# Optimization experiments

Measured on AMD Instinct MI355X. Metric: run time of the kernel, lower is better.

## Reference

```python
import jax, jax.numpy as jnp
import numpy as np

B, L, H = 2, 4096, 1024
ED, N, R, K = 2048, 16, 64, 4


def setup_inputs() -> dict:
    key = jax.random.key(0)
    ks = jax.random.split(key, 8)
    w = lambda i, shape, s=0.02: jax.random.normal(ks[i], shape, jnp.float32) * s
    # dt bias initialized like Mamba: inv-softplus of dt ~ logU(1e-3, 1e-1)
    dt = jnp.exp(jax.random.uniform(ks[7], (ED,)) * (np.log(0.1) - np.log(0.001)) + np.log(0.001))
    dt = jnp.clip(dt, 1e-4)
    inv_dt = dt + jnp.log(-jnp.expm1(-dt))
    A = jnp.broadcast_to(jnp.arange(1, N + 1, dtype=jnp.float32), (ED, N))
    return dict(
        x=jax.random.normal(ks[0], (B, L, H), jnp.float32),
        in_proj_w=w(1, (2 * ED, H)),
        conv_w=w(2, (ED, K), 0.2),
        conv_b=jnp.zeros((ED,), jnp.float32),
        x_proj_w=w(3, (R + 2 * N, ED)),
        dt_w=w(4, (ED, R), 64 ** -0.5),
        dt_b=inv_dt,
        A_log=jnp.log(A),
        D=jnp.ones((ED,), jnp.float32),
        out_proj_w=w(5, (H, ED)),
    )


def reference(x, in_proj_w, conv_w, conv_b, x_proj_w, dt_w, dt_b, A_log, D, out_proj_w):
    Bq, Lq, Hq = x.shape
    EDq, Kq = conv_w.shape
    Rq = dt_w.shape[1]
    Nq = A_log.shape[1]

    # in_proj -> [B, L, 2*ED]; chunk into hidden_states and gate
    xz = jnp.einsum('blh,eh->ble', x, in_proj_w)
    hs, gate = jnp.split(xz, 2, axis=-1)

    # causal depthwise conv1d along L (padding K-1 on the left), then SiLU
    hs_pad = jnp.pad(hs, ((0, 0), (Kq - 1, 0), (0, 0)))  # [B, L+K-1, ED]
    conv = conv_b
    for k in range(Kq):  # K=4, fixed small loop
        conv = conv + hs_pad[:, k:k + Lq, :] * conv_w[:, k]
    hs = jax.nn.silu(conv)  # [B, L, ED]

    # x_proj -> split into dt (rank R), B (N), C (N)
    ssm = jnp.einsum('ble,pe->blp', hs, x_proj_w)
    dtr, Bm, Cm = jnp.split(ssm, [Rq, Rq + Nq], axis=-1)

    # dt_proj + softplus (delta_softplus=True with delta_bias)
    delta = jax.nn.softplus(jnp.einsum('blr,er->ble', dtr, dt_w) + dt_b)  # [B,L,ED]

    A = -jnp.exp(A_log)  # [ED, N]

    # selective scan: h_t = exp(delta_t*A)*h_{t-1} + delta_t*B_t*u_t ; y_t = <h_t, C_t>
    def step(h, inp):
        d_t, B_t, C_t, u_t = inp  # [B,ED], [B,N], [B,N], [B,ED]
        dA = jnp.exp(d_t[..., None] * A)                      # [B,ED,N]
        h = dA * h + (d_t * u_t)[..., None] * B_t[:, None, :]  # [B,ED,N]
        y = jnp.einsum('ben,bn->be', h, C_t)                   # [B,ED]
        return h, y

    h0 = jnp.zeros((Bq, EDq, Nq), x.dtype)
    xs = (jnp.moveaxis(delta, 1, 0), jnp.moveaxis(Bm, 1, 0),
          jnp.moveaxis(Cm, 1, 0), jnp.moveaxis(hs, 1, 0))
    _, ys = jax.lax.scan(step, h0, xs)  # ys: [L, B, ED]

    y = jnp.moveaxis(ys, 0, 1) + hs * D      # skip term D*u
    y = y * jax.nn.silu(gate)                # gated output
    return jnp.einsum('ble,he->blh', y, out_proj_w)
```

## Files before the change

### kernel.cpp

```cpp
#include <hip/hip_runtime.h>


typedef float f32x4 __attribute__((ext_vector_type(4)));
typedef short short8 __attribute__((ext_vector_type(8)));

#define DEV __device__ __forceinline__

DEV float bf2f(unsigned short u) {
  union { unsigned int i; float f; } v; v.i = ((unsigned int)u) << 16; return v.f;
}
DEV unsigned short f2bf(float f) {
  union { float f; unsigned int i; } v; v.f = f;
  return (unsigned short)((v.i + 0x7fffu + ((v.i >> 16) & 1u)) >> 16);
}

DEV void gload_lds16(const void* g, void* l) {
  __builtin_amdgcn_global_load_lds(
      (const __attribute__((address_space(1))) unsigned int*)g,
      (__attribute__((address_space(3))) unsigned int*)l, 16, 0, 0);
}

DEV void mfma_bf16(f32x4& d, short8 a, short8 b) {
  asm("v_mfma_f32_16x16x32_bf16 %0, %1, %2, %0" : "+v"(d) : "v"(a), "v"(b));
}

template <int BM, int BN, int WM, int WN, int EPI>
__global__ __launch_bounds__(256) void gemm_bt_kernel(
    const unsigned short* __restrict__ A, const unsigned short* __restrict__ Bw,
    int M, int N, int Kd,
    float* __restrict__ o_f32, unsigned short* __restrict__ o_b16a,
    unsigned short* __restrict__ o_b16b, const float* __restrict__ bias,
    float* __restrict__ oB, float* __restrict__ oC)
{
  constexpr int MFR = BM / WM / 16;
  constexpr int NFR = BN / WN / 16;
  constexpr int TA = BM * 4;
  constexpr int TB = BN * 4;
  __shared__ unsigned short lds[(BM + BN) * 32];

  const int tid  = threadIdx.x;
  const int wave = tid >> 6;
  const int lane = tid & 63;
  const int row  = lane & 15;
  const int g    = lane >> 4;
  const int swz  = g ^ ((row >> 1) & 3);
  const int rowBase = blockIdx.y * BM;
  const int colBase = blockIdx.x * BN;
  const int WROW = (wave / WN) * (BM / WM);
  const int WCOL = (wave % WN) * (BN / WN);

  f32x4 acc[MFR][NFR];
  const f32x4 fz = {0.f, 0.f, 0.f, 0.f};
#pragma unroll
  for (int i = 0; i < MFR; ++i)
#pragma unroll
    for (int j = 0; j < NFR; ++j) acc[i][j] = fz;

  for (int kk = 0; kk < Kd; kk += 32) {
#pragma unroll
    for (int c0 = 0; c0 < TA; c0 += 256) {
      int ch = c0 + tid;
      if (ch < TA) {
        int r = ch >> 2;
        int gs = (ch & 3) ^ ((r >> 1) & 3);
        gload_lds16(A + (size_t)(rowBase + r) * Kd + kk + gs * 8,
                    (void*)(lds + (c0 + wave * 64) * 8));
      }
    }
#pragma unroll
    for (int c0 = 0; c0 < TB; c0 += 256) {
      int ch = c0 + tid;
      if (ch < TB) {
        int r = ch >> 2;
        int gs = (ch & 3) ^ ((r >> 1) & 3);
        gload_lds16(Bw + (size_t)(colBase + r) * Kd + kk + gs * 8,
                    (void*)(lds + BM * 32 + (c0 + wave * 64) * 8));
      }
    }
    __syncthreads();
    short8 af[MFR], bfr[NFR];
#pragma unroll
    for (int mi = 0; mi < MFR; ++mi)
      af[mi] = *(const short8*)(lds + (WROW + mi * 16 + row) * 32 + swz * 8);
#pragma unroll
    for (int ni = 0; ni < NFR; ++ni)
      bfr[ni] = *(const short8*)(lds + BM * 32 + (WCOL + ni * 16 + row) * 32 + swz * 8);
#pragma unroll
    for (int mi = 0; mi < MFR; ++mi)
#pragma unroll
      for (int ni = 0; ni < NFR; ++ni)
        mfma_bf16(acc[mi][ni], af[mi], bfr[ni]);
    __syncthreads();
  }

#pragma unroll
  for (int mi = 0; mi < MFR; ++mi) {
#pragma unroll
    for (int ni = 0; ni < NFR; ++ni) {
      const int gcol = colBase + WCOL + ni * 16 + row;
#pragma unroll
      for (int r = 0; r < 4; ++r) {
        const int grow = rowBase + WROW + mi * 16 + g * 4 + r;
        float v = acc[mi][ni][r];
        if constexpr (EPI == 0) {
          o_f32[(size_t)grow * N + gcol] = v;
        } else if constexpr (EPI == 1) {
          if (gcol < 2048) o_b16a[(size_t)grow * 2048 + gcol] = f2bf(v);
          else             o_b16b[(size_t)grow * 2048 + (gcol - 2048)] = f2bf(v);
        } else if constexpr (EPI == 2) {
          if (gcol < 64)      o_b16a[(size_t)grow * 64 + gcol] = f2bf(v);
          else if (gcol < 80) oB[(size_t)grow * 16 + (gcol - 64)] = v;
          else                oC[(size_t)grow * 16 + (gcol - 80)] = v;
        } else {
          float x = v + bias[gcol];
          o_f32[(size_t)grow * N + gcol] = (x > 20.f) ? x : __logf(1.f + __expf(x));
        }
      }
    }
  }
}

__global__ __launch_bounds__(256) void cvt_bf16_kernel(
    const float* __restrict__ in, unsigned short* __restrict__ out, int n8)
{
  int i = blockIdx.x * 256 + threadIdx.x;
  if (i >= n8) return;
  const float4* p = (const float4*)(in + (size_t)i * 8);
  float4 a = p[0], b = p[1];
  float v[8] = {a.x, a.y, a.z, a.w, b.x, b.y, b.z, b.w};
  unsigned o[4];
#pragma unroll
  for (int q = 0; q < 4; ++q)
    o[q] = (unsigned)f2bf(v[2 * q]) | ((unsigned)f2bf(v[2 * q + 1]) << 16);
  *(uint4*)(out + (size_t)i * 8) = make_uint4(o[0], o[1], o[2], o[3]);
}

__global__ __launch_bounds__(256) void conv_silu_kernel(
    const unsigned short* __restrict__ hsraw, const float* __restrict__ cw,
    const float* __restrict__ cb, unsigned short* __restrict__ hsb)
{
  int idx = blockIdx.x * 256 + threadIdx.x;
  int e0 = (idx & 255) * 8;
  int t  = (idx >> 8) & 4095;
  int b  = idx >> 20;
  float acc[8];
  float wv[4][8];
#pragma unroll
  for (int j = 0; j < 8; ++j) acc[j] = cb[e0 + j];
#pragma unroll
  for (int k = 0; k < 4; ++k)
#pragma unroll
    for (int j = 0; j < 8; ++j) wv[k][j] = cw[(e0 + j) * 4 + k];
#pragma unroll
  for (int k = 0; k < 4; ++k) {
    int tt = t - 3 + k;
    if (tt < 0) continue;
    uint4 v4 = *(const uint4*)(hsraw + ((size_t)(b * 4096 + tt)) * 2048 + e0);
    unsigned arr[4] = {v4.x, v4.y, v4.z, v4.w};
#pragma unroll
    for (int q = 0; q < 4; ++q) {
      acc[2 * q]     += wv[k][2 * q]     * bf2f((unsigned short)(arr[q] & 0xffffu));
      acc[2 * q + 1] += wv[k][2 * q + 1] * bf2f((unsigned short)(arr[q] >> 16));
    }
  }
  unsigned o[4];
#pragma unroll
  for (int q = 0; q < 4; ++q) {
    float a0 = acc[2 * q], a1 = acc[2 * q + 1];
    a0 = a0 / (1.f + __expf(-a0));
    a1 = a1 / (1.f + __expf(-a1));
    o[q] = (unsigned)f2bf(a0) | ((unsigned)f2bf(a1) << 16);
  }
  *(uint4*)(hsb + ((size_t)(b * 4096 + t)) * 2048 + e0) = make_uint4(o[0], o[1], o[2], o[3]);
}

__global__ __launch_bounds__(256) void scan_phase1(
    const float* __restrict__ delta, const unsigned short* __restrict__ hsb,
    const float* __restrict__ Bb, const float* __restrict__ alog,
    float* __restrict__ h_end, float* __restrict__ Ssum)
{
  __shared__ __align__(16) float Bs[64 * 16];
  const int tid = threadIdx.x;
  const int e = blockIdx.x * 256 + tid;
  const int c = blockIdx.y;
  const int b = blockIdx.z;
  const int t0 = c * 64;
  {
    const float* src = Bb + ((size_t)(b * 4096 + t0)) * 16;
#pragma unroll
    for (int k = 0; k < 4; ++k) Bs[tid + k * 256] = src[tid + k * 256];
  }
  float An[16];
  {
    const float4* ap = (const float4*)(alog + e * 16);
#pragma unroll
    for (int q = 0; q < 4; ++q) {
      float4 v = ap[q];
      An[4*q+0] = -__expf(v.x); An[4*q+1] = -__expf(v.y);
      An[4*q+2] = -__expf(v.z); An[4*q+3] = -__expf(v.w);
    }
  }
  __syncthreads();
  float h[16];
#pragma unroll
  for (int n = 0; n < 16; ++n) h[n] = 0.f;
  float sumd = 0.f;
  size_t base = ((size_t)(b * 4096 + t0)) * 2048 + e;
  float dd = delta[base];
  float uu = bf2f(hsb[base]);
  for (int j = 0; j < 64; ++j) {
    int jn = (j < 63) ? j + 1 : 63;
    float d_nxt = delta[base + (size_t)jn * 2048];
    float u_nxt = bf2f(hsb[base + (size_t)jn * 2048]);
    const float4* Bv = (const float4*)(Bs + j * 16);
    float4 b0 = Bv[0], b1 = Bv[1], b2 = Bv[2], b3 = Bv[3];
    float Bl[16] = {b0.x,b0.y,b0.z,b0.w, b1.x,b1.y,b1.z,b1.w,
                    b2.x,b2.y,b2.z,b2.w, b3.x,b3.y,b3.z,b3.w};
    sumd += dd;
    float du = dd * uu;
#pragma unroll
    for (int n = 0; n < 16; ++n)
      h[n] = fmaf(__expf(An[n] * dd), h[n], du * Bl[n]);
    dd = d_nxt; uu = u_nxt;
  }
  float* he = h_end + (((size_t)(b * 2048 + e)) * 64 + c) * 16;
#pragma unroll
  for (int q = 0; q < 4; ++q) {
    float4 v = {h[4*q], h[4*q+1], h[4*q+2], h[4*q+3]};
    *(float4*)(he + 4 * q) = v;
  }
  Ssum[((size_t)(b * 2048 + e)) * 64 + c] = sumd;
}

__global__ __launch_bounds__(256) void scan_phase2(
    const float* __restrict__ h_end, const float* __restrict__ Ssum,
    const float* __restrict__ alog, float* __restrict__ h_start)
{
  const int tid = threadIdx.x;
  const int n = tid & 15;
  const int G = blockIdx.x * 16 + (tid >> 4);
  const int e = G & 2047;
  const float An = -__expf(alog[e * 16 + n]);
  size_t hb = (size_t)G * 64 * 16 + n;
  size_t sb = (size_t)G * 64;
  float h = 0.f;
  constexpr int PF = 8;
  float hq[PF], Sq[PF];
#pragma unroll
  for (int j = 0; j < PF; ++j) { hq[j] = h_end[hb + (size_t)j * 16]; Sq[j] = Ssum[sb + j]; }
  for (int c0 = 0; c0 < 64; c0 += PF) {
    float hn[PF], Sn[PF];
#pragma unroll
    for (int j = 0; j < PF; ++j) {
      int cn = c0 + PF + j; cn = (cn < 64) ? cn : 63;
      hn[j] = h_end[hb + (size_t)cn * 16]; Sn[j] = Ssum[sb + cn];
    }
#pragma unroll
    for (int j = 0; j < PF; ++j) {
      h_start[hb + (size_t)(c0 + j) * 16] = h;
      h = fmaf(__expf(An * Sq[j]), h, hq[j]);
    }
#pragma unroll
    for (int j = 0; j < PF; ++j) { hq[j] = hn[j]; Sq[j] = Sn[j]; }
  }
}

__global__ __launch_bounds__(256) void scan_phase3(
    const float* __restrict__ delta, const unsigned short* __restrict__ hsb,
    const float* __restrict__ Bb, const float* __restrict__ Cb,
    const float* __restrict__ alog, const float* __restrict__ h_start,
    const float* __restrict__ Dv, unsigned short* __restrict__ gate_y2)
{
  __shared__ __align__(16) float Bs[64 * 16];
  __shared__ __align__(16) float Cs[64 * 16];
  const int tid = threadIdx.x;
  const int e = blockIdx.x * 256 + tid;
  const int c = blockIdx.y;
  const int b = blockIdx.z;
  const int t0 = c * 64;
  {
    const float* srcB = Bb + ((size_t)(b * 4096 + t0)) * 16;
    const float* srcC = Cb + ((size_t)(b * 4096 + t0)) * 16;
#pragma unroll
    for (int k = 0; k < 4; ++k) {
      Bs[tid + k * 256] = srcB[tid + k * 256];
      Cs[tid + k * 256] = srcC[tid + k * 256];
    }
  }
  float An[16];
  {
    const float4* ap = (const float4*)(alog + e * 16);
#pragma unroll
    for (int q = 0; q < 4; ++q) {
      float4 v = ap[q];
      An[4*q+0] = -__expf(v.x); An[4*q+1] = -__expf(v.y);
      An[4*q+2] = -__expf(v.z); An[4*q+3] = -__expf(v.w);
    }
  }
  const float De = Dv[e];
  float h[16];
  {
    const float4* hp = (const float4*)(h_start + (((size_t)(b * 2048 + e)) * 64 + c) * 16);
#pragma unroll
    for (int q = 0; q < 4; ++q) {
      float4 v = hp[q];
      h[4*q+0] = v.x; h[4*q+1] = v.y; h[4*q+2] = v.z; h[4*q+3] = v.w;
    }
  }
  __syncthreads();
  size_t base = ((size_t)(b * 4096 + t0)) * 2048 + e;
  float dd = delta[base];
  float uu = bf2f(hsb[base]);
  float gg = bf2f(gate_y2[base]);
  for (int j = 0; j < 64; ++j) {
    int jn = (j < 63) ? j + 1 : 63;
    float d_nxt = delta[base + (size_t)jn * 2048];
    float u_nxt = bf2f(hsb[base + (size_t)jn * 2048]);
    float g_nxt = bf2f(gate_y2[base + (size_t)jn * 2048]);
    const float4* Bv = (const float4*)(Bs + j * 16);
    const float4* Cv = (const float4*)(Cs + j * 16);
    float4 b0 = Bv[0], b1 = Bv[1], b2 = Bv[2], b3 = Bv[3];
    float4 c0v = Cv[0], c1v = Cv[1], c2v = Cv[2], c3v = Cv[3];
    float Bl[16] = {b0.x,b0.y,b0.z,b0.w, b1.x,b1.y,b1.z,b1.w,
                    b2.x,b2.y,b2.z,b2.w, b3.x,b3.y,b3.z,b3.w};
    float Cl[16] = {c0v.x,c0v.y,c0v.z,c0v.w, c1v.x,c1v.y,c1v.z,c1v.w,
                    c2v.x,c2v.y,c2v.z,c2v.w, c3v.x,c3v.y,c3v.z,c3v.w};
    float du = dd * uu;
    float y = 0.f;
#pragma unroll
    for (int n = 0; n < 16; ++n) {
      h[n] = fmaf(__expf(An[n] * dd), h[n], du * Bl[n]);
      y = fmaf(h[n], Cl[n], y);
    }
    float val = (y + uu * De) * (gg / (1.f + __expf(-gg)));
    gate_y2[base + (size_t)j * 2048] = f2bf(val);
    dd = d_nxt; uu = u_nxt; gg = g_nxt;
  }
}

extern "C" void kernel_launch(void* const* d_in, const int* in_sizes, int n_in,
                              void* d_out, int out_size, void* d_ws, size_t ws_size,
                              hipStream_t stream)
{
  const float* x    = (const float*)d_in[0];
  const float* w1   = (const float*)d_in[1];
  const float* cw   = (const float*)d_in[2];
  const float* cb   = (const float*)d_in[3];
  const float* xp   = (const float*)d_in[4];
  const float* dtw  = (const float*)d_in[5];
  const float* dtb  = (const float*)d_in[6];
  const float* alog = (const float*)d_in[7];
  const float* Dp   = (const float*)d_in[8];
  const float* wo   = (const float*)d_in[9];
  float* out = (float*)d_out;
  char* ws = (char*)d_ws;

  const size_t o_xb    = 0;
  const size_t o_wb1   = 16777216;
  const size_t o_xpb   = 25165824;
  const size_t o_dtwb  = 25559040;
  const size_t o_wob   = 25821184;
  const size_t o_hsraw = 30015488;
  const size_t o_gate  = 63569920;
  const size_t o_hsb   = 97124352;
  const size_t o_dtrb  = 130678784;
  const size_t o_Bb    = 131727360;
  const size_t o_Cb    = 132251648;
  const size_t o_delta = 132775936;
  const size_t WS_NEED = o_delta + 67108864 + 262144;
  if (ws_size < WS_NEED) return;

  unsigned short* xb    = (unsigned short*)(ws + o_xb);
  unsigned short* wb1   = (unsigned short*)(ws + o_wb1);
  unsigned short* xpb   = (unsigned short*)(ws + o_xpb);
  unsigned short* dtwb  = (unsigned short*)(ws + o_dtwb);
  unsigned short* wob   = (unsigned short*)(ws + o_wob);
  unsigned short* hsraw = (unsigned short*)(ws + o_hsraw);
  unsigned short* gate  = (unsigned short*)(ws + o_gate);
  unsigned short* hsb   = (unsigned short*)(ws + o_hsb);
  unsigned short* dtrb  = (unsigned short*)(ws + o_dtrb);
  float* Bb    = (float*)(ws + o_Bb);
  float* Cb    = (float*)(ws + o_Cb);
  float* delta = (float*)(ws + o_delta);
  float* h_end   = (float*)(ws + o_xb);
  float* h_start = (float*)(ws + o_hsraw);
  float* Ssum    = (float*)(ws + o_hsraw + 16777216);

  cvt_bf16_kernel<<<4096, 256, 0, stream>>>(x,   xb,   1048576);
  cvt_bf16_kernel<<<2048, 256, 0, stream>>>(w1,  wb1,  524288);
  cvt_bf16_kernel<<<96,   256, 0, stream>>>(xp,  xpb,  24576);
  cvt_bf16_kernel<<<64,   256, 0, stream>>>(dtw, dtwb, 16384);
  cvt_bf16_kernel<<<1024, 256, 0, stream>>>(wo,  wob,  262144);

  gemm_bt_kernel<128,128,2,2,1><<<dim3(32,64), 256, 0, stream>>>(
      xb, wb1, 8192, 4096, 1024, nullptr, hsraw, gate, nullptr, nullptr, nullptr);
  conv_silu_kernel<<<8192, 256, 0, stream>>>(hsraw, cw, cb, hsb);
  gemm_bt_kernel<64,96,4,1,2><<<dim3(1,128), 256, 0, stream>>>(
      hsb, xpb, 8192, 96, 2048, nullptr, dtrb, nullptr, nullptr, Bb, Cb);
  gemm_bt_kernel<64,64,2,2,3><<<dim3(32,128), 256, 0, stream>>>(
      dtrb, dtwb, 8192, 2048, 64, delta, nullptr, nullptr, dtb, nullptr, nullptr);

  scan_phase1<<<dim3(8, 64, 2), 256, 0, stream>>>(delta, hsb, Bb, alog, h_end, Ssum);
  scan_phase2<<<256, 256, 0, stream>>>(h_end, Ssum, alog, h_start);
  scan_phase3<<<dim3(8, 64, 2), 256, 0, stream>>>(
      delta, hsb, Bb, Cb, alog, h_start, Dp, gate);

  gemm_bt_kernel<128,128,2,2,0><<<dim3(8,64), 256, 0, stream>>>(
      gate, wob, 8192, 1024, 2048, out, nullptr, nullptr, nullptr, nullptr, nullptr);
}
```

Measured before the change: 394.8 us.

## Store delta in bf16, add BK=64 GEMM tiles, merge weight conversions

The delta produced by the dt_proj GEMM is now stored as bf16 instead of fp32, which halves the delta write traffic and the reads in both scan phases. The GEMM template gains a BK parameter with a matching XOR swizzle. BK=64 is used for in_proj and x_proj, and x_proj also gets smaller row tiles so more blocks run. The four weight fp32-to-bf16 conversions are merged into one launch. Storing delta in bf16 loses precision in the scan's exp(delta*A) and in the delta*u term.

```diff
diff --git a/kernel.cpp b/kernel.cpp
--- a/kernel.cpp
+++ b/kernel.cpp
@@ -3,15 +3,16 @@
 
 typedef float f32x4 __attribute__((ext_vector_type(4)));
 typedef short short8 __attribute__((ext_vector_type(8)));
+typedef unsigned short u16;
 
 #define DEV __device__ __forceinline__
 
-DEV float bf2f(unsigned short u) {
+DEV float bf2f(u16 u) {
   union { unsigned int i; float f; } v; v.i = ((unsigned int)u) << 16; return v.f;
 }
-DEV unsigned short f2bf(float f) {
+DEV u16 f2bf(float f) {
   union { float f; unsigned int i; } v; v.f = f;
-  return (unsigned short)((v.i + 0x7fffu + ((v.i >> 16) & 1u)) >> 16);
+  return (u16)((v.i + 0x7fffu + ((v.i >> 16) & 1u)) >> 16);
 }
 
 DEV void gload_lds16(const void* g, void* l) {
@@ -24,45 +25,48 @@
   asm("v_mfma_f32_16x16x32_bf16 %0, %1, %2, %0" : "+v"(d) : "v"(a), "v"(b));
 }
 
-template <int BM, int BN, int WM, int WN, int EPI>
+template <int BM, int BN, int WM, int WN, int BK, int EPI>
 __global__ __launch_bounds__(256) void gemm_bt_kernel(
-    const unsigned short* __restrict__ A, const unsigned short* __restrict__ Bw,
+    const u16* __restrict__ A, const u16* __restrict__ Bw,
     int M, int N, int Kd,
-    float* __restrict__ o_f32, unsigned short* __restrict__ o_b16a,
-    unsigned short* __restrict__ o_b16b, const float* __restrict__ bias,
+    float* __restrict__ o_f32, u16* __restrict__ o_b16a,
+    u16* __restrict__ o_b16b, const float* __restrict__ bias,
     float* __restrict__ oB, float* __restrict__ oC)
 {
+  constexpr int KSN = BK / 32;
+  constexpr int CPR = BK / 8;
+  constexpr int CPL = (CPR == 8) ? 3 : 2;
   constexpr int MFR = BM / WM / 16;
   constexpr int NFR = BN / WN / 16;
-  constexpr int TA = BM * 4;
-  constexpr int TB = BN * 4;
-  __shared__ unsigned short lds[(BM + BN) * 32];
+  constexpr int TA = BM * CPR;
+  constexpr int TB = BN * CPR;
+  __shared__ u16 lds[(BM + BN) * BK];
 
   const int tid  = threadIdx.x;
   const int wave = tid >> 6;
   const int lane = tid & 63;
   const int row  = lane & 15;
   const int g    = lane >> 4;
-  const int swz  = g ^ ((row >> 1) & 3);
+  const int key  = (CPR == 8) ? (row & 7) : ((row >> 1) & 3);
   const int rowBase = blockIdx.y * BM;
   const int colBase = blockIdx.x * BN;
   const int WROW = (wave / WN) * (BM / WM);
   const int WCOL = (wave % WN) * (BN / WN);
 
   f32x4 acc[MFR][NFR];
-  const f32x4 fz = {0.f, 0.f, 0.f, 0.f};
 #pragma unroll
   for (int i = 0; i < MFR; ++i)
 #pragma unroll
-    for (int j = 0; j < NFR; ++j) acc[i][j] = fz;
-
-  for (int kk = 0; kk < Kd; kk += 32) {
+    for (int j = 0; j < NFR; ++j) acc[i][j] = (f32x4){0.f, 0.f, 0.f, 0.f};
+
+  for (int kk = 0; kk < Kd; kk += BK) {
 #pragma unroll
     for (int c0 = 0; c0 < TA; c0 += 256) {
       int ch = c0 + tid;
       if (ch < TA) {
-        int r = ch >> 2;
-        int gs = (ch & 3) ^ ((r >> 1) & 3);
+        int r = ch >> CPL;
+        int rk = (CPR == 8) ? (r & 7) : ((r >> 1) & 3);
+        int gs = (ch & (CPR - 1)) ^ rk;
         gload_lds16(A + (size_t)(rowBase + r) * Kd + kk + gs * 8,
                     (void*)(lds + (c0 + wave * 64) * 8));
       }
@@ -71,25 +75,34 @@
     for (int c0 = 0; c0 < TB; c0 += 256) {
       int ch = c0 + tid;
       if (ch < TB) {
-        int r = ch >> 2;
-        int gs = (ch & 3) ^ ((r >> 1) & 3);
+        int r = ch >> CPL;
+        int rk = (CPR == 8) ? (r & 7) : ((r >> 1) & 3);
+        int gs = (ch & (CPR - 1)) ^ rk;
         gload_lds16(Bw + (size_t)(colBase + r) * Kd + kk + gs * 8,
-                    (void*)(lds + BM * 32 + (c0 + wave * 64) * 8));
+                    (void*)(lds + BM * BK + (c0 + wave * 64) * 8));
       }
     }
     __syncthreads();
-    short8 af[MFR], bfr[NFR];
+    short8 af[MFR][KSN], bfr[NFR][KSN];
 #pragma unroll
     for (int mi = 0; mi < MFR; ++mi)
-      af[mi] = *(const short8*)(lds + (WROW + mi * 16 + row) * 32 + swz * 8);
+#pragma unroll
+      for (int ks = 0; ks < KSN; ++ks)
+        af[mi][ks] = *(const short8*)(lds + (WROW + mi * 16 + row) * BK +
+                                      (((ks * 4 + g) ^ key) * 8));
 #pragma unroll
     for (int ni = 0; ni < NFR; ++ni)
-      bfr[ni] = *(const short8*)(lds + BM * 32 + (WCOL + ni * 16 + row) * 32 + swz * 8);
-#pragma unroll
-    for (int mi = 0; mi < MFR; ++mi)
-#pragma unroll
-      for (int ni = 0; ni < NFR; ++ni)
-        mfma_bf16(acc[mi][ni], af[mi], bfr[ni]);
+#pragma unroll
+      for (int ks = 0; ks < KSN; ++ks)
+        bfr[ni][ks] = *(const short8*)(lds + BM * BK + (WCOL + ni * 16 + row) * BK +
+                                       (((ks * 4 + g) ^ key) * 8));
+#pragma unroll
+    for (int ks = 0; ks < KSN; ++ks)
+#pragma unroll
+      for (int mi = 0; mi < MFR; ++mi)
+#pragma unroll
+        for (int ni = 0; ni < NFR; ++ni)
+          mfma_bf16(acc[mi][ni], af[mi][ks], bfr[ni][ks]);
     __syncthreads();
   }
 
@@ -113,31 +126,52 @@
           else                oC[(size_t)grow * 16 + (gcol - 80)] = v;
         } else {
           float x = v + bias[gcol];
-          o_f32[(size_t)grow * N + gcol] = (x > 20.f) ? x : __logf(1.f + __expf(x));
+          float sp = (x > 20.f) ? x : __logf(1.f + __expf(x));
+          o_b16a[(size_t)grow * N + gcol] = f2bf(sp);
         }
       }
     }
   }
 }
 
-__global__ __launch_bounds__(256) void cvt_bf16_kernel(
-    const float* __restrict__ in, unsigned short* __restrict__ out, int n8)
-{
-  int i = blockIdx.x * 256 + threadIdx.x;
-  if (i >= n8) return;
-  const float4* p = (const float4*)(in + (size_t)i * 8);
+DEV void cvt8(const float* in, u16* out, int j) {
+  const float4* p = (const float4*)(in + (size_t)j * 8);
   float4 a = p[0], b = p[1];
   float v[8] = {a.x, a.y, a.z, a.w, b.x, b.y, b.z, b.w};
   unsigned o[4];
 #pragma unroll
   for (int q = 0; q < 4; ++q)
     o[q] = (unsigned)f2bf(v[2 * q]) | ((unsigned)f2bf(v[2 * q + 1]) << 16);
-  *(uint4*)(out + (size_t)i * 8) = make_uint4(o[0], o[1], o[2], o[3]);
+  *(uint4*)(out + (size_t)j * 8) = make_uint4(o[0], o[1], o[2], o[3]);
+}
+
+__global__ __launch_bounds__(256) void cvt_bf16_kernel(
+    const float* __restrict__ in, u16* __restrict__ out, int n8)
+{
+  int i = blockIdx.x * 256 + threadIdx.x;
+  if (i >= n8) return;
+  cvt8(in, out, i);
+}
+
+__global__ __launch_bounds__(256) void cvt4_kernel(
+    const float* __restrict__ a0, u16* __restrict__ o0, int n0,
+    const float* __restrict__ a1, u16* __restrict__ o1, int n1,
+    const float* __restrict__ a2, u16* __restrict__ o2, int n2,
+    const float* __restrict__ a3, u16* __restrict__ o3, int n3)
+{
+  int i = blockIdx.x * 256 + threadIdx.x;
+  if (i < n0)                { cvt8(a0, o0, i); return; }
+  i -= n0;
+  if (i < n1)                { cvt8(a1, o1, i); return; }
+  i -= n1;
+  if (i < n2)                { cvt8(a2, o2, i); return; }
+  i -= n2;
+  if (i < n3)                { cvt8(a3, o3, i); }
 }
 
 __global__ __launch_bounds__(256) void conv_silu_kernel(
-    const unsigned short* __restrict__ hsraw, const float* __restrict__ cw,
-    const float* __restrict__ cb, unsigned short* __restrict__ hsb)
+    const u16* __restrict__ hsraw, const float* __restrict__ cw,
+    const float* __restrict__ cb, u16* __restrict__ hsb)
 {
   int idx = blockIdx.x * 256 + threadIdx.x;
   int e0 = (idx & 255) * 8;
@@ -159,8 +193,8 @@
     unsigned arr[4] = {v4.x, v4.y, v4.z, v4.w};
 #pragma unroll
     for (int q = 0; q < 4; ++q) {
-      acc[2 * q]     += wv[k][2 * q]     * bf2f((unsigned short)(arr[q] & 0xffffu));
-      acc[2 * q + 1] += wv[k][2 * q + 1] * bf2f((unsigned short)(arr[q] >> 16));
+      acc[2 * q]     += wv[k][2 * q]     * bf2f((u16)(arr[q] & 0xffffu));
+      acc[2 * q + 1] += wv[k][2 * q + 1] * bf2f((u16)(arr[q] >> 16));
     }
   }
   unsigned o[4];
@@ -175,7 +209,7 @@
 }
 
 __global__ __launch_bounds__(256) void scan_phase1(
-    const float* __restrict__ delta, const unsigned short* __restrict__ hsb,
+    const u16* __restrict__ deltab, const u16* __restrict__ hsb,
     const float* __restrict__ Bb, const float* __restrict__ alog,
     float* __restrict__ h_end, float* __restrict__ Ssum)
 {
@@ -206,11 +240,11 @@
   for (int n = 0; n < 16; ++n) h[n] = 0.f;
   float sumd = 0.f;
   size_t base = ((size_t)(b * 4096 + t0)) * 2048 + e;
-  float dd = delta[base];
+  float dd = bf2f(deltab[base]);
   float uu = bf2f(hsb[base]);
   for (int j = 0; j < 64; ++j) {
     int jn = (j < 63) ? j + 1 : 63;
-    float d_nxt = delta[base + (size_t)jn * 2048];
+    float d_nxt = bf2f(deltab[base + (size_t)jn * 2048]);
     float u_nxt = bf2f(hsb[base + (size_t)jn * 2048]);
     const float4* Bv = (const float4*)(Bs + j * 16);
     float4 b0 = Bv[0], b1 = Bv[1], b2 = Bv[2], b3 = Bv[3];
@@ -266,10 +300,10 @@
 }
 
 __global__ __launch_bounds__(256) void scan_phase3(
-    const float* __restrict__ delta, const unsigned short* __restrict__ hsb,
+    const u16* __restrict__ deltab, const u16* __restrict__ hsb,
     const float* __restrict__ Bb, const float* __restrict__ Cb,
     const float* __restrict__ alog, const float* __restrict__ h_start,
-    const float* __restrict__ Dv, unsigned short* __restrict__ gate_y2)
+    const float* __restrict__ Dv, u16* __restrict__ gate_y2)
 {
   __shared__ __align__(16) float Bs[64 * 16];
   __shared__ __align__(16) float Cs[64 * 16];
@@ -309,12 +343,12 @@
   }
   __syncthreads();
   size_t base = ((size_t)(b * 4096 + t0)) * 2048 + e;
-  float dd = delta[base];
+  float dd = bf2f(deltab[base]);
   float uu = bf2f(hsb[base]);
   float gg = bf2f(gate_y2[base]);
   for (int j = 0; j < 64; ++j) {
     int jn = (j < 63) ? j + 1 : 63;
-    float d_nxt = delta[base + (size_t)jn * 2048];
+    float d_nxt = bf2f(deltab[base + (size_t)jn * 2048]);
     float u_nxt = bf2f(hsb[base + (size_t)jn * 2048]);
     float g_nxt = bf2f(gate_y2[base + (size_t)jn * 2048]);
     const float4* Bv = (const float4*)(Bs + j * 16);
@@ -370,41 +404,39 @@
   const size_t WS_NEED = o_delta + 67108864 + 262144;
   if (ws_size < WS_NEED) return;
 
-  unsigned short* xb    = (unsigned short*)(ws + o_xb);
-  unsigned short* wb1   = (unsigned short*)(ws + o_wb1);
-  unsigned short* xpb   = (unsigned short*)(ws + o_xpb);
-  unsigned short* dtwb  = (unsigned short*)(ws + o_dtwb);
-  unsigned short* wob   = (unsigned short*)(ws + o_wob);
-  unsigned short* hsraw = (unsigned short*)(ws + o_hsraw);
-  unsigned short* gate  = (unsigned short*)(ws + o_gate);
-  unsigned short* hsb   = (unsigned short*)(ws + o_hsb);
-  unsigned short* dtrb  = (unsigned short*)(ws + o_dtrb);
+  u16* xb    = (u16*)(ws + o_xb);
+  u16* wb1   = (u16*)(ws + o_wb1);
+  u16* xpb   = (u16*)(ws + o_xpb);
+  u16* dtwb  = (u16*)(ws + o_dtwb);
+  u16* wob   = (u16*)(ws + o_wob);
+  u16* hsraw = (u16*)(ws + o_hsraw);
+  u16* gate  = (u16*)(ws + o_gate);
+  u16* hsb   = (u16*)(ws + o_hsb);
+  u16* dtrb  = (u16*)(ws + o_dtrb);
   float* Bb    = (float*)(ws + o_Bb);
   float* Cb    = (float*)(ws + o_Cb);
-  float* delta = (float*)(ws + o_delta);
+  u16* deltab  = (u16*)(ws + o_delta);
   float* h_end   = (float*)(ws + o_xb);
   float* h_start = (float*)(ws + o_hsraw);
   float* Ssum    = (float*)(ws + o_hsraw + 16777216);
 
-  cvt_bf16_kernel<<<4096, 256, 0, stream>>>(x,   xb,   1048576);
-  cvt_bf16_kernel<<<2048, 256, 0, stream>>>(w1,  wb1,  524288);
-  cvt_bf16_kernel<<<96,   256, 0, stream>>>(xp,  xpb,  24576);
-  cvt_bf16_kernel<<<64,   256, 0, stream>>>(dtw, dtwb, 16384);
-  cvt_bf16_kernel<<<1024, 256, 0, stream>>>(wo,  wob,  262144);
-
-  gemm_bt_kernel<128,128,2,2,1><<<dim3(32,64), 256, 0, stream>>>(
+  cvt_bf16_kernel<<<4096, 256, 0, stream>>>(x, xb, 1048576);
+  cvt4_kernel<<<3232, 256, 0, stream>>>(
+      w1, wb1, 524288, xp, xpb, 24576, dtw, dtwb, 16384, wo, wob, 262144);
+
+  gemm_bt_kernel<128,128,2,2,64,1><<<dim3(32,64), 256, 0, stream>>>(
       xb, wb1, 8192, 4096, 1024, nullptr, hsraw, gate, nullptr, nullptr, nullptr);
   conv_silu_kernel<<<8192, 256, 0, stream>>>(hsraw, cw, cb, hsb);
-  gemm_bt_kernel<64,96,4,1,2><<<dim3(1,128), 256, 0, stream>>>(
+  gemm_bt_kernel<32,96,2,2,64,2><<<dim3(1,256), 256, 0, stream>>>(
       hsb, xpb, 8192, 96, 2048, nullptr, dtrb, nullptr, nullptr, Bb, Cb);
-  gemm_bt_kernel<64,64,2,2,3><<<dim3(32,128), 256, 0, stream>>>(
-      dtrb, dtwb, 8192, 2048, 64, delta, nullptr, nullptr, dtb, nullptr, nullptr);
-
-  scan_phase1<<<dim3(8, 64, 2), 256, 0, stream>>>(delta, hsb, Bb, alog, h_end, Ssum);
+  gemm_bt_kernel<64,64,2,2,32,3><<<dim3(32,128), 256, 0, stream>>>(
+      dtrb, dtwb, 8192, 2048, 64, nullptr, deltab, nullptr, dtb, nullptr, nullptr);
+
+  scan_phase1<<<dim3(8, 64, 2), 256, 0, stream>>>(deltab, hsb, Bb, alog, h_end, Ssum);
   scan_phase2<<<256, 256, 0, stream>>>(h_end, Ssum, alog, h_start);
   scan_phase3<<<dim3(8, 64, 2), 256, 0, stream>>>(
-      delta, hsb, Bb, Cb, alog, h_start, Dp, gate);
-
-  gemm_bt_kernel<128,128,2,2,0><<<dim3(8,64), 256, 0, stream>>>(
+      deltab, hsb, Bb, Cb, alog, h_start, Dp, gate);
+
+  gemm_bt_kernel<128,128,2,2,32,0><<<dim3(8,64), 256, 0, stream>>>(
       gate, wob, 8192, 1024, 2048, out, nullptr, nullptr, nullptr, nullptr, nullptr);
 }
```

New measurement: 379.8 us. -3.8%, faster.
